# Kernel tuning notes

Hardware: AMD Instinct MI355X
Metric: run time of the kernel (lower is better)

The kernel has to match this reference:

```python
import jax, jax.numpy as jnp
import numpy as np

CE_TEMP = 1.0
SIMW_TEMP = 0.1
NSEG = 2048
EPS = 1e-8
NEG = jnp.float32(-1e30)


def setup_inputs() -> dict:
    key = jax.random.key(0)
    k1, k2, k3, k4, k5, k6 = jax.random.split(key, 6)
    N, C, H, W, Ch, S = 2, 19, 128, 128, 256, NSEG
    inputs_plbl = jax.random.normal(k1, (N, C, H, W), dtype=jnp.float32)
    feats_plbl = jax.random.normal(k2, (N, Ch, H, W), dtype=jnp.float32)
    inputs = jax.random.normal(k3, (N, C, H, W), dtype=jnp.float32)
    # multi-hot targets per superpixel; ~2.3 active classes on average -> many multi-hot rows
    targets = jax.random.bernoulli(k4, 0.12, (N, S, C)).astype(jnp.float32)
    superpixels = jax.random.randint(k5, (N, H, W), 0, S, dtype=jnp.int32)
    spmasks = jax.random.bernoulli(k6, 0.5, (N, H, W))
    return {"inputs_plbl": inputs_plbl, "feats_plbl": feats_plbl, "inputs": inputs,
            "targets": targets, "superpixels": superpixels, "spmasks": spmasks}


def _per_image(out_plbl, feat, out, trg_table, sp, mask):
    # out_plbl: [HW,C] softmax'd pseudo-label probs; feat: [HW,Ch]; out: [HW,C];
    # trg_table: [S,C] multi-hot; sp: [HW] int superpixel ids; mask: [HW] bool
    HW, C = out_plbl.shape
    S = trg_table.shape[0]
    trg_pix = trg_table[sp]                                  # [HW,C]
    multi_spx = trg_table.sum(-1) > 1.0                      # [S]
    valid = mask & multi_spx[sp]                             # == spmask & multi-hot mask

    # scatter_max: argmax pixel per (superpixel, class) among valid pixels
    scores = jnp.where(valid[:, None], out_plbl, NEG)
    seg_max = jax.ops.segment_max(scores, sp, num_segments=S)       # [S,C]
    is_max = valid[:, None] & (scores >= seg_max[sp])
    cand = jnp.where(is_max, jnp.arange(HW, dtype=jnp.int32)[:, None], HW)
    proto_idx = jax.ops.segment_min(cand, sp, num_segments=S)       # [S,C]
    proto_idx = jnp.clip(proto_idx, 0, HW - 1)

    # prototype features and per-pixel similarities to own-superpixel class prototypes
    proto_feat = feat[proto_idx]                             # [S,C,Ch]
    pf_pix = proto_feat[sp]                                  # [HW,C,Ch] (dominant intermediate)
    sim = jnp.einsum('kcd,kd->kc', pf_pix, feat) / SIMW_TEMP  # [HW,C]

    # scatter_softmax over the active classes of the pixel's superpixel
    active = trg_pix > 0.0
    w_multi = jax.nn.softmax(jnp.where(active, sim, NEG), axis=-1)
    w_row = jnp.where(active, w_multi, trg_pix)              # inactive entries keep 0
    w = jnp.where(valid[:, None], w_row, trg_pix)            # non-multi pixels keep one-hot
    w = jax.lax.stop_gradient(w)                             # original computes weights under no_grad

    ce = -jnp.log(out + EPS)                                 # [HW,C]
    contrib = jnp.where(mask[:, None], w * ce, 0.0)
    any_valid = jnp.any(valid)                               # image skipped if no multi-hot masked pixel
    loss_i = jnp.where(any_valid, contrib.sum(), 0.0)
    cnt_i = jnp.where(any_valid, mask.sum(), 0)
    return loss_i, cnt_i


def reference(inputs_plbl, feats_plbl, inputs, targets, superpixels, spmasks):
    N, C, H, W = inputs_plbl.shape
    Ch = feats_plbl.shape[1]
    out_plbl = jax.nn.softmax(inputs_plbl / CE_TEMP, axis=1).transpose(0, 2, 3, 1).reshape(N, -1, C)
    feats = feats_plbl.transpose(0, 2, 3, 1).reshape(N, -1, Ch)
    out = jax.nn.softmax(inputs / CE_TEMP, axis=1).transpose(0, 2, 3, 1).reshape(N, -1, C)
    sp = superpixels.reshape(N, -1)
    mask = spmasks.reshape(N, -1)
    loss_i, cnt_i = jax.vmap(_per_image)(out_plbl, feats, out, targets, sp, mask)
    total = loss_i.sum()
    cnt = cnt_i.sum()
    return jnp.where(cnt > 0, total / jnp.maximum(cnt, 1).astype(jnp.float32), 0.0)
```

## Files before the change

kernel.cpp:

```cpp
#include <hip/hip_runtime.h>
#include <cstdint>
#include <cstddef>

#define NN   2
#define CC   19
#define HWD  16384
#define CH   256
#define SS   2048
#define BCAP 32

#define EPSV 1e-8f

__global__ void k_multi(const float* __restrict__ trg, int* __restrict__ multi,
                        int* __restrict__ sp_cnt, float* __restrict__ slots,
                        int* __restrict__ cnt, int* __restrict__ vcnt) {
    int i = blockIdx.x * blockDim.x + threadIdx.x;
    if (i >= NN * SS) return;
    const float* t = trg + (size_t)i * CC;
    float s = 0.f;
    #pragma unroll
    for (int c = 0; c < CC; ++c) s += t[c];
    multi[i] = (s > 1.0f) ? 1 : 0;
    sp_cnt[i] = 0;
    if (i < 256) slots[i] = 0.f;
    if (i < 2) { cnt[i] = 0; vcnt[i] = 0; }
}

__global__ void k_softmax(const float* __restrict__ xp, const float* __restrict__ xi,
                          float* __restrict__ plbl_pm, float* __restrict__ ce_pm) {
    int gid = blockIdx.x * blockDim.x + threadIdx.x;
    int second = (gid >= NN * HWD);
    int idx = second ? gid - NN * HWD : gid;
    int n = idx >> 14;
    int k = idx & (HWD - 1);
    const float* src = (second ? xi : xp) + (size_t)n * CC * HWD + k;
    float v[CC];
    float m = -1e30f;
    #pragma unroll
    for (int c = 0; c < CC; ++c) { v[c] = src[(size_t)c * HWD]; m = fmaxf(m, v[c]); }
    float s = 0.f;
    #pragma unroll
    for (int c = 0; c < CC; ++c) { v[c] = expf(v[c] - m); s += v[c]; }
    float inv = 1.f / s;
    if (!second) {
        float* op = plbl_pm + (size_t)idx * CC;
        #pragma unroll
        for (int c = 0; c < CC; ++c) op[c] = v[c] * inv;
    } else {
        float* cp = ce_pm + (size_t)idx * CC;
        #pragma unroll
        for (int c = 0; c < CC; ++c) cp[c] = -logf(v[c] * inv + EPSV);
    }
}

__global__ void k_prep(const int* __restrict__ sp, const int* __restrict__ msk,
                       const int* __restrict__ multi, const float* __restrict__ trg,
                       const float* __restrict__ ce_pm, int* __restrict__ sp_cnt,
                       unsigned short* __restrict__ bucket,
                       unsigned char* __restrict__ validf,
                       int* __restrict__ cnt, int* __restrict__ vcnt,
                       float* __restrict__ slots) {
    int idx = blockIdx.x * blockDim.x + threadIdx.x;
    if (idx >= NN * HWD) return;
    int n = idx >> 14;
    int k = idx & (HWD - 1);
    int lane = threadIdx.x & 63;
    int m = (msk[idx] != 0);
    int s = sp[idx];
    int mu = multi[n * SS + s];
    int valid = m && mu;
    validf[idx] = (unsigned char)valid;
    unsigned long long mb = __ballot(m);
    unsigned long long vb = __ballot(valid);
    if (valid) {
        int cell = n * SS + s;
        int pos = atomicAdd(&sp_cnt[cell], 1);
        if (pos < BCAP) bucket[(size_t)cell * BCAP + pos] = (unsigned short)k;
    }
    float contrib = 0.f;
    if (m && !mu) {
        const float* t  = trg + ((size_t)n * SS + s) * CC;
        const float* ce = ce_pm + (size_t)idx * CC;
        #pragma unroll
        for (int c = 0; c < CC; ++c) contrib += t[c] * ce[c];
    }
    #pragma unroll
    for (int off = 32; off >= 1; off >>= 1) contrib += __shfl_xor(contrib, off);
    if (lane == 0) {
        if (mb) atomicAdd(&cnt[n], __popcll(mb));
        if (vb) atomicAdd(&vcnt[n], __popcll(vb));
        if (contrib != 0.f) atomicAdd(&slots[n * 128 + ((idx >> 6) & 127)], contrib);
    }
}

__global__ void k_transpose(const float* __restrict__ F,
                            const unsigned char* __restrict__ validf,
                            float* __restrict__ FT) {
    __shared__ float tile[64][65];
    __shared__ unsigned char vld[64];
    int n  = blockIdx.z;
    int k0 = blockIdx.x * 64;
    int d0 = blockIdx.y * 64;
    const float* src = F + (size_t)n * CH * HWD;
    float* dst = FT + (size_t)n * HWD * CH;
    int tx = threadIdx.x, ty = threadIdx.y;
    if (ty == 0) vld[tx] = validf[n * HWD + k0 + tx];
    #pragma unroll
    for (int i = 0; i < 16; ++i) {
        int dd = ty + 4 * i;
        tile[dd][tx] = src[(size_t)(d0 + dd) * HWD + (k0 + tx)];
    }
    __syncthreads();
    #pragma unroll
    for (int i = 0; i < 16; ++i) {
        int kk = ty + 4 * i;
        if (vld[kk]) dst[(size_t)(k0 + kk) * CH + (d0 + tx)] = tile[tx][kk];
    }
}

__global__ __launch_bounds__(256) void k_argmax(
        const float* __restrict__ plbl_pm, const int* __restrict__ sp_cnt,
        const unsigned short* __restrict__ bucket, const int* __restrict__ multi,
        unsigned short* __restrict__ proto) {
    int id   = (blockIdx.x * blockDim.x + threadIdx.x) >> 6;
    int lane = threadIdx.x & 63;
    if (id >= NN * SS) return;
    if (!multi[id]) return;
    int cnt = sp_cnt[id];
    if (cnt == 0) return;
    cnt = min(cnt, BCAP);
    int n = id >> 11;
    int my_pix = (lane < cnt) ? (int)bucket[(size_t)id * BCAP + lane] : 0;
    float bv = -1e30f;
    int   bi = HWD;
    for (int i = 0; i < cnt; ++i) {
        int pix = __shfl(my_pix, i);
        if (lane < CC) {
            float v = plbl_pm[((size_t)(n * HWD + pix)) * CC + lane];
            if (v > bv || (v == bv && pix < bi)) { bv = v; bi = pix; }
        }
    }
    if (lane < CC) proto[(size_t)id * CC + lane] = (unsigned short)bi;
}

__global__ __launch_bounds__(256) void k_simloss(
        const float* __restrict__ feat_t, const float* __restrict__ ce_pm,
        const float* __restrict__ trg, const int* __restrict__ sp_cnt,
        const unsigned short* __restrict__ bucket, const int* __restrict__ multi,
        const unsigned short* __restrict__ proto, float* __restrict__ slots) {
    int id = blockIdx.x;
    if (!multi[id]) return;
    int cnt = sp_cnt[id];
    if (cnt == 0) return;
    cnt = min(cnt, BCAP);
    int n    = id >> 11;
    int tid  = threadIdx.x;
    int lane = tid & 63;
    int wv   = tid >> 6;

    __shared__ float protoF[CC][CH];
    __shared__ int   actc[CC];
    __shared__ int   s_nact;

    if (tid < 64) {
        float t = (lane < CC) ? trg[(size_t)id * CC + lane] : 0.f;
        unsigned long long act = __ballot(t > 0.f);
        int pos = __popcll(act & ((1ull << lane) - 1ull));
        if (t > 0.f) actc[pos] = lane;
        if (lane == 0) s_nact = __popcll(act);
    }
    __syncthreads();
    int nact = s_nact;
    for (int a = wv; a < nact; a += 4) {
        int p = proto[(size_t)id * CC + actc[a]];
        float4 v = ((const float4*)(feat_t + ((size_t)(n * HWD + p)) * CH))[lane];
        ((float4*)(&protoF[a][0]))[lane] = v;
    }
    __syncthreads();

    float wcontrib = 0.f;
    for (int i = wv; i < cnt; i += 4) {
        int pix = bucket[(size_t)id * BCAP + i];
        float4 f = ((const float4*)(feat_t + ((size_t)(n * HWD + pix)) * CH))[lane];
        float mysim = -1e30f;
        for (int a = 0; a < nact; ++a) {
            float4 pf = ((const float4*)(&protoF[a][0]))[lane];
            float d = f.x * pf.x + f.y * pf.y + f.z * pf.z + f.w * pf.w;
            #pragma unroll
            for (int off = 32; off >= 1; off >>= 1) d += __shfl_xor(d, off);
            if (lane == a) mysim = d * 10.0f;
        }
        float mx = mysim;
        #pragma unroll
        for (int off = 32; off >= 1; off >>= 1) mx = fmaxf(mx, __shfl_xor(mx, off));
        float e = (lane < nact) ? expf(mysim - mx) : 0.f;
        float se = e;
        #pragma unroll
        for (int off = 32; off >= 1; off >>= 1) se += __shfl_xor(se, off);
        float ce = (lane < nact)
                 ? ce_pm[((size_t)(n * HWD + pix)) * CC + actc[lane]] : 0.f;
        float c1 = (e / se) * ce;
        #pragma unroll
        for (int off = 32; off >= 1; off >>= 1) c1 += __shfl_xor(c1, off);
        wcontrib += c1;
    }
    if (lane == 0 && wcontrib != 0.f)
        atomicAdd(&slots[n * 128 + (id & 127)], wcontrib);
}

__global__ void k_final(const float* __restrict__ slots, const int* __restrict__ cnt,
                        const int* __restrict__ vcnt, float* __restrict__ out) {
    __shared__ float red[2];
    int t = threadIdx.x;
    int w = t >> 6;
    int lane = t & 63;
    float v = slots[w * 128 + lane] + slots[w * 128 + lane + 64];
    #pragma unroll
    for (int off = 32; off >= 1; off >>= 1) v += __shfl_xor(v, off);
    if (lane == 0) red[w] = v;
    __syncthreads();
    if (t == 0) {
        float total = 0.f;
        int c = 0;
        for (int n = 0; n < NN; ++n)
            if (vcnt[n] > 0) { total += red[n]; c += cnt[n]; }
        out[0] = (c > 0) ? total / (float)c : 0.f;
    }
}

extern "C" void kernel_launch(void* const* d_in, const int* in_sizes, int n_in,
                              void* d_out, int out_size, void* d_ws, size_t ws_size,
                              hipStream_t stream) {
    const float* inputs_plbl = (const float*)d_in[0];
    const float* feats_plbl  = (const float*)d_in[1];
    const float* inputs      = (const float*)d_in[2];
    const float* targets     = (const float*)d_in[3];
    const int*   superpixels = (const int*)d_in[4];
    const int*   spmasks     = (const int*)d_in[5];
    float* out = (float*)d_out;

    char* ws = (char*)d_ws;
    int*   sp_cnt = (int*)ws;
    int*   cnt    = (int*)(ws + 16384);
    int*   vcnt   = (int*)(ws + 16392);
    float* slots  = (float*)(ws + 16416);
    unsigned char*  validf = (unsigned char*)(ws + 17440);
    unsigned short* bucket = (unsigned short*)(ws + 50208);
    unsigned short* proto  = (unsigned short*)(ws + 312352);
    int*   multi  = (int*)(ws + 468000);
    float* plbl_pm = (float*)(ws + 484384);
    float* ce_pm   = (float*)(ws + 2974752);
    float* feat_t  = (float*)(ws + 5465120);

    k_multi<<<(NN * SS + 255) / 256, 256, 0, stream>>>(targets, multi, sp_cnt,
                                                       slots, cnt, vcnt);
    k_softmax<<<(2 * NN * HWD) / 256, 256, 0, stream>>>(inputs_plbl, inputs,
                                                        plbl_pm, ce_pm);
    k_prep<<<(NN * HWD) / 256, 256, 0, stream>>>(superpixels, spmasks, multi,
                                                 targets, ce_pm, sp_cnt, bucket,
                                                 validf, cnt, vcnt, slots);
    dim3 tg(HWD / 64, CH / 64, NN);
    k_transpose<<<tg, dim3(64, 4), 0, stream>>>(feats_plbl, validf, feat_t);
    k_argmax<<<(NN * SS * 64) / 256, 256, 0, stream>>>(plbl_pm, sp_cnt, bucket,
                                                       multi, proto);
    k_simloss<<<NN * SS, 256, 0, stream>>>(feat_t, ce_pm, targets, sp_cnt,
                                           bucket, multi, proto, slots);
    k_final<<<1, 128, 0, stream>>>(slots, cnt, vcnt, out);
}
```

Measured before the change: 146.0 us.

## Fuse softmax into prep kernel and argmax into similarity kernel

Merges the softmax pass into the per-pixel prep kernel. Softmax is now computed only for masked pixels, and pseudo-label probabilities are written only for valid ones. Non-multi-hot pixels take their cross-entropy term directly instead of reading it back from global memory. The per-superpixel argmax is folded into the similarity kernel, with prototype indices kept in shared memory. This removes two launches and the round trips through the global proto and full plbl/ce buffers. In exchange, each similarity block does a serial argmax in one wave, and the fused kernel has more branch divergence and register pressure.

```diff
diff --git a/kernel.cpp b/kernel.cpp
--- a/kernel.cpp
+++ b/kernel.cpp
@@ -26,42 +26,15 @@
     if (i < 2) { cnt[i] = 0; vcnt[i] = 0; }
 }
 
-__global__ void k_softmax(const float* __restrict__ xp, const float* __restrict__ xi,
-                          float* __restrict__ plbl_pm, float* __restrict__ ce_pm) {
-    int gid = blockIdx.x * blockDim.x + threadIdx.x;
-    int second = (gid >= NN * HWD);
-    int idx = second ? gid - NN * HWD : gid;
-    int n = idx >> 14;
-    int k = idx & (HWD - 1);
-    const float* src = (second ? xi : xp) + (size_t)n * CC * HWD + k;
-    float v[CC];
-    float m = -1e30f;
-    #pragma unroll
-    for (int c = 0; c < CC; ++c) { v[c] = src[(size_t)c * HWD]; m = fmaxf(m, v[c]); }
-    float s = 0.f;
-    #pragma unroll
-    for (int c = 0; c < CC; ++c) { v[c] = expf(v[c] - m); s += v[c]; }
-    float inv = 1.f / s;
-    if (!second) {
-        float* op = plbl_pm + (size_t)idx * CC;
-        #pragma unroll
-        for (int c = 0; c < CC; ++c) op[c] = v[c] * inv;
-    } else {
-        float* cp = ce_pm + (size_t)idx * CC;
-        #pragma unroll
-        for (int c = 0; c < CC; ++c) cp[c] = -logf(v[c] * inv + EPSV);
-    }
-}
-
-__global__ void k_prep(const int* __restrict__ sp, const int* __restrict__ msk,
-                       const int* __restrict__ multi, const float* __restrict__ trg,
-                       const float* __restrict__ ce_pm, int* __restrict__ sp_cnt,
-                       unsigned short* __restrict__ bucket,
-                       unsigned char* __restrict__ validf,
-                       int* __restrict__ cnt, int* __restrict__ vcnt,
-                       float* __restrict__ slots) {
+__global__ __launch_bounds__(256) void k_main(
+        const float* __restrict__ xp, const float* __restrict__ xi,
+        const float* __restrict__ trg, const int* __restrict__ sp,
+        const int* __restrict__ msk, const int* __restrict__ multi,
+        int* __restrict__ sp_cnt, unsigned short* __restrict__ bucket,
+        unsigned char* __restrict__ validf, float* __restrict__ plbl_pm,
+        float* __restrict__ ce_pm, int* __restrict__ cnt,
+        int* __restrict__ vcnt, float* __restrict__ slots) {
     int idx = blockIdx.x * blockDim.x + threadIdx.x;
-    if (idx >= NN * HWD) return;
     int n = idx >> 14;
     int k = idx & (HWD - 1);
     int lane = threadIdx.x & 63;
@@ -72,17 +45,45 @@
     validf[idx] = (unsigned char)valid;
     unsigned long long mb = __ballot(m);
     unsigned long long vb = __ballot(valid);
+
     if (valid) {
         int cell = n * SS + s;
         int pos = atomicAdd(&sp_cnt[cell], 1);
         if (pos < BCAP) bucket[(size_t)cell * BCAP + pos] = (unsigned short)k;
-    }
+        const float* a = xp + (size_t)n * CC * HWD + k;
+        float v[CC];
+        float mx = -1e30f;
+        #pragma unroll
+        for (int c = 0; c < CC; ++c) { v[c] = a[(size_t)c * HWD]; mx = fmaxf(mx, v[c]); }
+        float su = 0.f;
+        #pragma unroll
+        for (int c = 0; c < CC; ++c) { v[c] = expf(v[c] - mx); su += v[c]; }
+        float inv = 1.f / su;
+        float* op = plbl_pm + (size_t)idx * CC;
+        #pragma unroll
+        for (int c = 0; c < CC; ++c) op[c] = v[c] * inv;
+    }
+
     float contrib = 0.f;
-    if (m && !mu) {
-        const float* t  = trg + ((size_t)n * SS + s) * CC;
-        const float* ce = ce_pm + (size_t)idx * CC;
-        #pragma unroll
-        for (int c = 0; c < CC; ++c) contrib += t[c] * ce[c];
+    if (m) {
+        const float* b = xi + (size_t)n * CC * HWD + k;
+        float v[CC];
+        float mx = -1e30f;
+        #pragma unroll
+        for (int c = 0; c < CC; ++c) { v[c] = b[(size_t)c * HWD]; mx = fmaxf(mx, v[c]); }
+        float su = 0.f;
+        #pragma unroll
+        for (int c = 0; c < CC; ++c) { v[c] = expf(v[c] - mx); su += v[c]; }
+        float inv = 1.f / su;
+        if (mu) {
+            float* cp = ce_pm + (size_t)idx * CC;
+            #pragma unroll
+            for (int c = 0; c < CC; ++c) cp[c] = -logf(v[c] * inv + EPSV);
+        } else {
+            const float* t = trg + ((size_t)n * SS + s) * CC;
+            #pragma unroll
+            for (int c = 0; c < CC; ++c) contrib += t[c] * (-logf(v[c] * inv + EPSV));
+        }
     }
     #pragma unroll
     for (int off = 32; off >= 1; off >>= 1) contrib += __shfl_xor(contrib, off);
@@ -118,36 +119,11 @@
     }
 }
 
-__global__ __launch_bounds__(256) void k_argmax(
-        const float* __restrict__ plbl_pm, const int* __restrict__ sp_cnt,
-        const unsigned short* __restrict__ bucket, const int* __restrict__ multi,
-        unsigned short* __restrict__ proto) {
-    int id   = (blockIdx.x * blockDim.x + threadIdx.x) >> 6;
-    int lane = threadIdx.x & 63;
-    if (id >= NN * SS) return;
-    if (!multi[id]) return;
-    int cnt = sp_cnt[id];
-    if (cnt == 0) return;
-    cnt = min(cnt, BCAP);
-    int n = id >> 11;
-    int my_pix = (lane < cnt) ? (int)bucket[(size_t)id * BCAP + lane] : 0;
-    float bv = -1e30f;
-    int   bi = HWD;
-    for (int i = 0; i < cnt; ++i) {
-        int pix = __shfl(my_pix, i);
-        if (lane < CC) {
-            float v = plbl_pm[((size_t)(n * HWD + pix)) * CC + lane];
-            if (v > bv || (v == bv && pix < bi)) { bv = v; bi = pix; }
-        }
-    }
-    if (lane < CC) proto[(size_t)id * CC + lane] = (unsigned short)bi;
-}
-
-__global__ __launch_bounds__(256) void k_simloss(
+__global__ __launch_bounds__(256) void k_sim(
         const float* __restrict__ feat_t, const float* __restrict__ ce_pm,
-        const float* __restrict__ trg, const int* __restrict__ sp_cnt,
-        const unsigned short* __restrict__ bucket, const int* __restrict__ multi,
-        const unsigned short* __restrict__ proto, float* __restrict__ slots) {
+        const float* __restrict__ plbl_pm, const float* __restrict__ trg,
+        const int* __restrict__ sp_cnt, const unsigned short* __restrict__ bucket,
+        const int* __restrict__ multi, float* __restrict__ slots) {
     int id = blockIdx.x;
     if (!multi[id]) return;
     int cnt = sp_cnt[id];
@@ -159,28 +135,40 @@
     int wv   = tid >> 6;
 
     __shared__ float protoF[CC][CH];
+    __shared__ int   s_proto[CC];
     __shared__ int   actc[CC];
-    __shared__ int   s_nact;
-
-    if (tid < 64) {
-        float t = (lane < CC) ? trg[(size_t)id * CC + lane] : 0.f;
-        unsigned long long act = __ballot(t > 0.f);
-        int pos = __popcll(act & ((1ull << lane) - 1ull));
-        if (t > 0.f) actc[pos] = lane;
-        if (lane == 0) s_nact = __popcll(act);
-    }
-    __syncthreads();
-    int nact = s_nact;
+
+    float t = (lane < CC) ? trg[(size_t)id * CC + lane] : 0.f;
+    unsigned long long act = __ballot(t > 0.f);
+    int nact = __popcll(act);
+    int apos = __popcll(act & ((1ull << lane) - 1ull));
+    if ((act >> lane) & 1ull) actc[apos] = lane;
+    int mypix = (lane < cnt) ? (int)bucket[(size_t)id * BCAP + lane] : 0;
+
+    if (wv == 0) {
+        float bv = -1e30f;
+        int   bi = HWD;
+        for (int i = 0; i < cnt; ++i) {
+            int pix = __shfl(mypix, i);
+            if (lane < CC) {
+                float v = plbl_pm[((size_t)(n * HWD + pix)) * CC + lane];
+                if (v > bv || (v == bv && pix < bi)) { bv = v; bi = pix; }
+            }
+        }
+        if ((act >> lane) & 1ull) s_proto[apos] = bi;
+    }
+    __syncthreads();
+
     for (int a = wv; a < nact; a += 4) {
-        int p = proto[(size_t)id * CC + actc[a]];
-        float4 v = ((const float4*)(feat_t + ((size_t)(n * HWD + p)) * CH))[lane];
-        ((float4*)(&protoF[a][0]))[lane] = v;
+        int p = s_proto[a];
+        ((float4*)(&protoF[a][0]))[lane] =
+            ((const float4*)(feat_t + ((size_t)(n * HWD + p)) * CH))[lane];
     }
     __syncthreads();
 
     float wcontrib = 0.f;
     for (int i = wv; i < cnt; i += 4) {
-        int pix = bucket[(size_t)id * BCAP + i];
+        int pix = __shfl(mypix, i);
         float4 f = ((const float4*)(feat_t + ((size_t)(n * HWD + pix)) * CH))[lane];
         float mysim = -1e30f;
         for (int a = 0; a < nact; ++a) {
@@ -246,24 +234,20 @@
     float* slots  = (float*)(ws + 16416);
     unsigned char*  validf = (unsigned char*)(ws + 17440);
     unsigned short* bucket = (unsigned short*)(ws + 50208);
-    unsigned short* proto  = (unsigned short*)(ws + 312352);
-    int*   multi  = (int*)(ws + 468000);
-    float* plbl_pm = (float*)(ws + 484384);
-    float* ce_pm   = (float*)(ws + 2974752);
-    float* feat_t  = (float*)(ws + 5465120);
+    int*   multi  = (int*)(ws + 312352);
+    float* plbl_pm = (float*)(ws + 328736);
+    float* ce_pm   = (float*)(ws + 2819104);
+    float* feat_t  = (float*)(ws + 5309472);
 
     k_multi<<<(NN * SS + 255) / 256, 256, 0, stream>>>(targets, multi, sp_cnt,
                                                        slots, cnt, vcnt);
-    k_softmax<<<(2 * NN * HWD) / 256, 256, 0, stream>>>(inputs_plbl, inputs,
-                                                        plbl_pm, ce_pm);
-    k_prep<<<(NN * HWD) / 256, 256, 0, stream>>>(superpixels, spmasks, multi,
-                                                 targets, ce_pm, sp_cnt, bucket,
-                                                 validf, cnt, vcnt, slots);
+    k_main<<<(NN * HWD) / 256, 256, 0, stream>>>(inputs_plbl, inputs, targets,
+                                                 superpixels, spmasks, multi,
+                                                 sp_cnt, bucket, validf,
+                                                 plbl_pm, ce_pm, cnt, vcnt, slots);
     dim3 tg(HWD / 64, CH / 64, NN);
     k_transpose<<<tg, dim3(64, 4), 0, stream>>>(feats_plbl, validf, feat_t);
-    k_argmax<<<(NN * SS * 64) / 256, 256, 0, stream>>>(plbl_pm, sp_cnt, bucket,
-                                                       multi, proto);
-    k_simloss<<<NN * SS, 256, 0, stream>>>(feat_t, ce_pm, targets, sp_cnt,
-                                           bucket, multi, proto, slots);
+    k_sim<<<NN * SS, 256, 0, stream>>>(feat_t, ce_pm, plbl_pm, targets,
+                                       sp_cnt, bucket, multi, slots);
     k_final<<<1, 128, 0, stream>>>(slots, cnt, vcnt, out);
 }
```

After: 136.0 us. 1.07x faster.
